# Optimization experiments

Hardware: AMD Instinct MI355X
Metric: run time of the kernel (lower is better)

Reference implementation:

```python
import jax, jax.numpy as jnp
import numpy as np

E = 8            # moe_num_experts
FFN = 8192       # ffn_hidden_size
D = 2048         # d_model
B, T = 1, 4096


def setup_inputs() -> dict:
    key = jax.random.key(0)
    k1, k2, k3, k4 = jax.random.split(key, 4)
    x = jax.random.normal(k1, (B, T, D), dtype=jnp.float32)
    # params stored flat as (E*FFN, D), as in the flax module
    w1 = jax.random.normal(k2, (E * FFN, D), dtype=jnp.float32) * 0.02
    v1 = jax.random.normal(k3, (E * FFN, D), dtype=jnp.float32) * 0.02
    w2 = jax.random.normal(k4, (E * FFN, D), dtype=jnp.float32) * 0.02
    return {"x": x, "w1": w1, "v1": v1, "w2": w2, "expert_idx": 3}


def reference(x, w1, v1, w2, expert_idx):
    # select this expert's weight slabs: (FFN, D) each
    expert_shape = (E, FFN, D)
    ew1 = w1.reshape(expert_shape)[expert_idx]
    ev1 = v1.reshape(expert_shape)[expert_idx]
    ew2 = w2.reshape(expert_shape)[expert_idx]
    # gate and up projections: [B,T,D] x [D,FFN] -> [B,T,FFN]
    x1 = jnp.einsum('btd,fd->btf', x, ew1)
    x2 = jnp.einsum('btd,fd->btf', x, ev1)
    h = jax.nn.silu(x1) * x2
    # down projection (note: matmul with ew2, i.e. contraction over FFN)
    out = jnp.einsum('btf,fd->btd', h, ew2)
    return out
```

## Files before the change

kernel.cpp:

```cpp
#include <hip/hip_runtime.h>

#define E_NUM 8
#define FFN_DIM 8192
#define D_DIM 2048
#define T_DIM 4096

using bf16x8 = __attribute__((ext_vector_type(8))) short;
using f32x4  = __attribute__((ext_vector_type(4))) float;
using u16x8  = __attribute__((ext_vector_type(8))) unsigned short;

__device__ __forceinline__ unsigned short f2bf(float f) {
  union { float f; unsigned int u; } v; v.f = f;
  unsigned int u = v.u;
  unsigned int r = (u + 0x7FFFu + ((u >> 16) & 1u)) >> 16;
  return (unsigned short)r;
}

__device__ __forceinline__ void gload16(const unsigned short* g, const unsigned short* l) {
  __builtin_amdgcn_global_load_lds(
      (const __attribute__((address_space(1))) void*)g,
      (__attribute__((address_space(3))) void*)l, 16, 0, 0);
}

__global__ void convert3_kernel(const float* __restrict__ x,
                                const float* __restrict__ w1,
                                const float* __restrict__ v1,
                                const int* __restrict__ eidx,
                                unsigned short* __restrict__ Xb,
                                unsigned short* __restrict__ W1b,
                                unsigned short* __restrict__ V1b) {
  const long slab = (long)FFN_DIM * D_DIM;
  const float* src;
  unsigned short* dst;
  long n;
  if (blockIdx.y == 0)      { src = w1 + (long)(*eidx) * slab; dst = W1b; n = slab; }
  else if (blockIdx.y == 1) { src = v1 + (long)(*eidx) * slab; dst = V1b; n = slab; }
  else                      { src = x;                          dst = Xb;  n = (long)T_DIM * D_DIM; }
  long stride = (long)gridDim.x * blockDim.x;
  for (long i = (long)blockIdx.x * blockDim.x + threadIdx.x; i * 8 < n; i += stride) {
    long e = i * 8;
    const float4* p = (const float4*)(src + e);
    float4 f0 = p[0], f1 = p[1];
    u16x8 o;
    o[0] = f2bf(f0.x); o[1] = f2bf(f0.y); o[2] = f2bf(f0.z); o[3] = f2bf(f0.w);
    o[4] = f2bf(f1.x); o[5] = f2bf(f1.y); o[6] = f2bf(f1.z); o[7] = f2bf(f1.w);
    *(u16x8*)(dst + e) = o;
  }
}

__global__ __launch_bounds__(512) void transpose_kernel(
    const float* __restrict__ w2, const int* __restrict__ eidx,
    unsigned short* __restrict__ dst) {
  __shared__ unsigned short tile[64][72];
  const float* src = w2 + (long)(*eidx) * (long)FFN_DIM * D_DIM;
  const int tid = threadIdx.x;
  int d0 = blockIdx.x << 6;
  int f0 = blockIdx.y << 6;
#pragma unroll
  for (int p = 0; p < 2; ++p) {
    int f = p * 32 + (tid >> 4);
    int dc = (tid & 15) * 4;
    float4 v = *(const float4*)(src + (long)(f0 + f) * D_DIM + d0 + dc);
    tile[f][dc + 0] = f2bf(v.x); tile[f][dc + 1] = f2bf(v.y);
    tile[f][dc + 2] = f2bf(v.z); tile[f][dc + 3] = f2bf(v.w);
  }
  __syncthreads();
  int d = tid >> 3;
  int fc = (tid & 7) * 8;
  u16x8 o;
#pragma unroll
  for (int j = 0; j < 8; ++j) o[j] = tile[fc + j][d];
  *(u16x8*)(dst + (long)(d0 + d) * FFN_DIM + f0 + fc) = o;
}

#define VMCNT6 asm volatile("s_waitcnt vmcnt(6)" ::: "memory")
#define VMCNT5 asm volatile("s_waitcnt vmcnt(5)" ::: "memory")
#define VMCNT3 asm volatile("s_waitcnt vmcnt(3)" ::: "memory")
#define VMCNT0 asm volatile("s_waitcnt vmcnt(0)" ::: "memory")
#define BAR asm volatile("s_waitcnt lgkmcnt(0)\n\ts_barrier" ::: "memory")
#define PRIO1 __builtin_amdgcn_s_setprio(1)
#define PRIO0 __builtin_amdgcn_s_setprio(0)

__global__ __launch_bounds__(512, 1) void gemm1_silu(
    const unsigned short* __restrict__ Xb,
    const unsigned short* __restrict__ W1b,
    const unsigned short* __restrict__ V1b,
    unsigned short* __restrict__ Hb) {
  __shared__ __align__(16) unsigned short sA[2 * 16384];
  __shared__ __align__(16) unsigned short sB1[2 * 8192];
  __shared__ __align__(16) unsigned short sB2[2 * 8192];

  const int tid = threadIdx.x;
  const int wv = tid >> 6, l = tid & 63;
  const int wm = wv >> 2, wn = wv & 3;
  const int kq = l >> 4, lr = l & 15;
  const int bsw = (blockIdx.x & 7) * 128 + (blockIdx.x >> 3);
  const int m0 = (bsw >> 6) << 8;
  const int n0 = (bsw & 63) << 7;

  const int rsub = tid >> 3;
  const int sslot8 = ((tid & 7) ^ ((tid >> 3) & 7)) << 3;
  const unsigned short* gA  = Xb  + (long)(m0 + rsub) * D_DIM + sslot8;
  const unsigned short* gB1 = W1b + (long)(n0 + rsub) * D_DIM + sslot8;
  const unsigned short* gB2 = V1b + (long)(n0 + rsub) * D_DIM + sslot8;

#define STG1(gbase, r_, tc_, lbase) \
  gload16((gbase) + (long)((r_) * 64) * D_DIM + (tc_), (lbase) + (r_) * 4096 + wv * 512)

  int aoffA[4], aoffB[4], boff[2];
#pragma unroll
  for (int j = 0; j < 4; ++j) {
    int rowA = wm * 64 + j * 16 + lr;
    aoffA[j] = rowA * 64 + ((kq ^ (rowA & 7)) << 3);
    int rowB = 128 + wm * 64 + j * 16 + lr;
    aoffB[j] = rowB * 64 + ((kq ^ (rowB & 7)) << 3);
  }
#pragma unroll
  for (int g = 0; g < 2; ++g) {
    int row = wn * 32 + g * 16 + lr;
    boff[g] = row * 64 + ((kq ^ (row & 7)) << 3);
  }

  f32x4 acc1[8][2], acc2[8][2];
  f32x4 z = {0.f, 0.f, 0.f, 0.f};
#pragma unroll
  for (int f = 0; f < 8; ++f)
#pragma unroll
    for (int g = 0; g < 2; ++g) { acc1[f][g] = z; acc2[f][g] = z; }

  bf16x8 aA[4][2], aB[4][2], b1[2][2], b2[2][2];

  STG1(gB1, 0, 0, sB1); STG1(gB1, 1, 0, sB1);
  STG1(gA, 0, 0, sA); STG1(gA, 1, 0, sA); STG1(gA, 2, 0, sA); STG1(gA, 3, 0, sA);
  STG1(gB2, 0, 0, sB2); STG1(gB2, 1, 0, sB2);
  STG1(gB1, 0, 64, sB1 + 8192); STG1(gB1, 1, 64, sB1 + 8192);
  STG1(gA, 0, 64, sA + 16384); STG1(gA, 1, 64, sA + 16384);
  STG1(gA, 2, 64, sA + 16384); STG1(gA, 3, 64, sA + 16384);
  STG1(gB2, 0, 64, sB2 + 8192); STG1(gB2, 1, 64, sB2 + 8192);
  asm volatile("s_waitcnt vmcnt(8)" ::: "memory");
  BAR;
#pragma unroll
  for (int j = 0; j < 4; ++j) {
    aA[j][0] = *(const bf16x8*)(sA + aoffA[j]);
    aA[j][1] = *(const bf16x8*)(sA + (aoffA[j] ^ 32));
  }
#pragma unroll
  for (int g = 0; g < 2; ++g) {
    b1[g][0] = *(const bf16x8*)(sB1 + boff[g]);
    b1[g][1] = *(const bf16x8*)(sB1 + (boff[g] ^ 32));
  }
  BAR;

  const int NT = D_DIM / 64;
  for (int t = 0; t < NT; ++t) {
    const int db = t & 1, nx = db ^ 1;
    const unsigned short* Acur  = sA  + db * 16384;
    const unsigned short* Anxt  = sA  + nx * 16384;
    const unsigned short* B1nxt = sB1 + nx * 8192;
    const unsigned short* B2cur = sB2 + db * 8192;
    unsigned short* AcurW  = (unsigned short*)sA  + db * 16384;
    unsigned short* B1curW = (unsigned short*)sB1 + db * 8192;
    unsigned short* B2curW = (unsigned short*)sB2 + db * 8192;
    const int p1ok = (t + 1 < NT), p2ok = (t + 2 < NT);
    const int tc2 = (t + 2) << 6;

#pragma unroll
    for (int j = 0; j < 4; ++j) {
      aB[j][0] = *(const bf16x8*)(Acur + aoffB[j]);
      aB[j][1] = *(const bf16x8*)(Acur + (aoffB[j] ^ 32));
    }
    if (p2ok) { STG1(gB1, 0, tc2, B1curW); STG1(gB1, 1, tc2, B1curW); }
    PRIO1;
#pragma unroll
    for (int j = 0; j < 4; ++j)
#pragma unroll
      for (int g = 0; g < 2; ++g) {
        acc1[j][g] = __builtin_amdgcn_mfma_f32_16x16x32_bf16(aA[j][0], b1[g][0], acc1[j][g], 0, 0, 0);
        acc1[j][g] = __builtin_amdgcn_mfma_f32_16x16x32_bf16(aA[j][1], b1[g][1], acc1[j][g], 0, 0, 0);
      }
    PRIO0;
    BAR;

#pragma unroll
    for (int g = 0; g < 2; ++g) {
      b2[g][0] = *(const bf16x8*)(B2cur + boff[g]);
      b2[g][1] = *(const bf16x8*)(B2cur + (boff[g] ^ 32));
    }
    if (p2ok) { STG1(gA, 0, tc2, AcurW); STG1(gA, 1, tc2, AcurW); STG1(gA, 2, tc2, AcurW); }
    PRIO1;
#pragma unroll
    for (int j = 0; j < 4; ++j)
#pragma unroll
      for (int g = 0; g < 2; ++g) {
        acc1[4 + j][g] = __builtin_amdgcn_mfma_f32_16x16x32_bf16(aB[j][0], b1[g][0], acc1[4 + j][g], 0, 0, 0);
        acc1[4 + j][g] = __builtin_amdgcn_mfma_f32_16x16x32_bf16(aB[j][1], b1[g][1], acc1[4 + j][g], 0, 0, 0);
      }
    PRIO0;
    if (p2ok) { VMCNT5; } else if (p1ok) { VMCNT0; }
    BAR;

    if (p2ok) { STG1(gA, 3, tc2, AcurW); STG1(gB2, 0, tc2, B2curW); STG1(gB2, 1, tc2, B2curW); }
    PRIO1;
#pragma unroll
    for (int j = 0; j < 4; ++j)
#pragma unroll
      for (int g = 0; g < 2; ++g) {
        acc2[j][g] = __builtin_amdgcn_mfma_f32_16x16x32_bf16(aA[j][0], b2[g][0], acc2[j][g], 0, 0, 0);
        acc2[j][g] = __builtin_amdgcn_mfma_f32_16x16x32_bf16(aA[j][1], b2[g][1], acc2[j][g], 0, 0, 0);
      }
    PRIO0;
    if (p1ok) {
#pragma unroll
      for (int j = 0; j < 4; ++j) {
        aA[j][0] = *(const bf16x8*)(Anxt + aoffA[j]);
        aA[j][1] = *(const bf16x8*)(Anxt + (aoffA[j] ^ 32));
      }
    }
    BAR;

    PRIO1;
#pragma unroll
    for (int j = 0; j < 4; ++j)
#pragma unroll
      for (int g = 0; g < 2; ++g) {
        acc2[4 + j][g] = __builtin_amdgcn_mfma_f32_16x16x32_bf16(aB[j][0], b2[g][0], acc2[4 + j][g], 0, 0, 0);
        acc2[4 + j][g] = __builtin_amdgcn_mfma_f32_16x16x32_bf16(aB[j][1], b2[g][1], acc2[4 + j][g], 0, 0, 0);
      }
    PRIO0;
    if (p1ok) {
#pragma unroll
      for (int g = 0; g < 2; ++g) {
        b1[g][0] = *(const bf16x8*)(B1nxt + boff[g]);
        b1[g][1] = *(const bf16x8*)(B1nxt + (boff[g] ^ 32));
      }
    }
    BAR;
  }

#pragma unroll
  for (int f = 0; f < 8; ++f)
#pragma unroll
    for (int g = 0; g < 2; ++g)
#pragma unroll
      for (int r = 0; r < 4; ++r) {
        int row = m0 + (f >> 2) * 128 + wm * 64 + (f & 3) * 16 + kq * 4 + r;
        int col = n0 + wn * 32 + g * 16 + lr;
        float x1 = acc1[f][g][r], x2 = acc2[f][g][r];
        float hv = x1 / (1.f + __expf(-x1)) * x2;
        Hb[(long)row * FFN_DIM + col] = f2bf(hv);
      }
#undef STG1
}

__global__ __launch_bounds__(512, 1) void gemm2(
    const unsigned short* __restrict__ Hb,
    const unsigned short* __restrict__ W2T,
    float* __restrict__ out) {
  __shared__ __align__(16) unsigned short sA[2 * 16384];
  __shared__ __align__(16) unsigned short sB[2 * 8192];

  const int tid = threadIdx.x;
  const int wv = tid >> 6, l = tid & 63;
  const int wm = wv >> 1, wn = wv & 1;
  const int kq = l >> 4, lr = l & 15;
  const int bsw = (blockIdx.x & 7) * 32 + (blockIdx.x >> 3);
  const int m0 = (bsw >> 4) << 8;
  const int n0 = (bsw & 15) << 7;

  const int rsub = tid >> 3;
  const int sslot8 = ((tid & 7) ^ ((tid >> 3) & 7)) << 3;
  const unsigned short* gA = Hb  + (long)(m0 + rsub) * FFN_DIM + sslot8;
  const unsigned short* gB = W2T + (long)(n0 + rsub) * FFN_DIM + sslot8;

#define STG1(gbase, r_, tc_, lbase) \
  gload16((gbase) + (long)((r_) * 64) * FFN_DIM + (tc_), (lbase) + (r_) * 4096 + wv * 512)

  int aoff[4], boff[4];
#pragma unroll
  for (int f = 0; f < 4; ++f) {
    int row = wm * 64 + f * 16 + lr;
    aoff[f] = row * 64 + ((kq ^ (row & 7)) << 3);
  }
#pragma unroll
  for (int g = 0; g < 4; ++g) {
    int row = wn * 64 + g * 16 + lr;
    boff[g] = row * 64 + ((kq ^ (row & 7)) << 3);
  }

  f32x4 acc[4][4];
  f32x4 z = {0.f, 0.f, 0.f, 0.f};
#pragma unroll
  for (int f = 0; f < 4; ++f)
#pragma unroll
    for (int g = 0; g < 4; ++g) acc[f][g] = z;

  bf16x8 aA[2][2], aB[2][2], bA[2][2], bB[2][2];

  STG1(gB, 0, 0, sB); STG1(gB, 1, 0, sB);
  STG1(gA, 0, 0, sA); STG1(gA, 1, 0, sA); STG1(gA, 2, 0, sA); STG1(gA, 3, 0, sA);
  STG1(gB, 0, 64, sB + 8192); STG1(gB, 1, 64, sB + 8192);
  STG1(gA, 0, 64, sA + 16384); STG1(gA, 1, 64, sA + 16384);
  STG1(gA, 2, 64, sA + 16384); STG1(gA, 3, 64, sA + 16384);
  VMCNT6;
  BAR;
#pragma unroll
  for (int f = 0; f < 2; ++f) {
    aA[f][0] = *(const bf16x8*)(sA + aoff[f]);
    aA[f][1] = *(const bf16x8*)(sA + (aoff[f] ^ 32));
  }
#pragma unroll
  for (int g = 0; g < 2; ++g) {
    bA[g][0] = *(const bf16x8*)(sB + boff[g]);
    bA[g][1] = *(const bf16x8*)(sB + (boff[g] ^ 32));
  }
  BAR;

  const int NT = FFN_DIM / 64;
  for (int t = 0; t < NT; ++t) {
    const int db = t & 1, nx = db ^ 1;
    const unsigned short* Acur = sA + db * 16384;
    const unsigned short* Anxt = sA + nx * 16384;
    const unsigned short* Bcur = sB + db * 8192;
    const unsigned short* Bnxt = sB + nx * 8192;
    unsigned short* AcurW = (unsigned short*)sA + db * 16384;
    unsigned short* BcurW = (unsigned short*)sB + db * 8192;
    const int p1ok = (t + 1 < NT), p2ok = (t + 2 < NT);
    const int tc2 = (t + 2) << 6;

#pragma unroll
    for (int f = 0; f < 2; ++f) {
      aB[f][0] = *(const bf16x8*)(Acur + aoff[2 + f]);
      aB[f][1] = *(const bf16x8*)(Acur + (aoff[2 + f] ^ 32));
    }
#pragma unroll
    for (int g = 0; g < 2; ++g) {
      bB[g][0] = *(const bf16x8*)(Bcur + boff[2 + g]);
      bB[g][1] = *(const bf16x8*)(Bcur + (boff[2 + g] ^ 32));
    }
    PRIO1;
#pragma unroll
    for (int f = 0; f < 2; ++f)
#pragma unroll
      for (int g = 0; g < 2; ++g) {
        acc[f][g] = __builtin_amdgcn_mfma_f32_16x16x32_bf16(aA[f][0], bA[g][0], acc[f][g], 0, 0, 0);
        acc[f][g] = __builtin_amdgcn_mfma_f32_16x16x32_bf16(aA[f][1], bA[g][1], acc[f][g], 0, 0, 0);
      }
    PRIO0;
    BAR;

    if (p2ok) { STG1(gB, 0, tc2, BcurW); STG1(gB, 1, tc2, BcurW); STG1(gA, 0, tc2, AcurW); }
    PRIO1;
#pragma unroll
    for (int f = 0; f < 2; ++f)
#pragma unroll
      for (int g = 0; g < 2; ++g) {
        acc[2 + f][g] = __builtin_amdgcn_mfma_f32_16x16x32_bf16(aB[f][0], bA[g][0], acc[2 + f][g], 0, 0, 0);
        acc[2 + f][g] = __builtin_amdgcn_mfma_f32_16x16x32_bf16(aB[f][1], bA[g][1], acc[2 + f][g], 0, 0, 0);
      }
    PRIO0;
    if (p2ok) { VMCNT3; } else if (p1ok) { VMCNT0; }
    BAR;

    if (p2ok) { STG1(gA, 1, tc2, AcurW); STG1(gA, 2, tc2, AcurW); STG1(gA, 3, tc2, AcurW); }
    PRIO1;
#pragma unroll
    for (int f = 0; f < 2; ++f)
#pragma unroll
      for (int g = 0; g < 2; ++g) {
        acc[f][2 + g] = __builtin_amdgcn_mfma_f32_16x16x32_bf16(aA[f][0], bB[g][0], acc[f][2 + g], 0, 0, 0);
        acc[f][2 + g] = __builtin_amdgcn_mfma_f32_16x16x32_bf16(aA[f][1], bB[g][1], acc[f][2 + g], 0, 0, 0);
      }
    PRIO0;
    if (p1ok) {
#pragma unroll
      for (int f = 0; f < 2; ++f) {
        aA[f][0] = *(const bf16x8*)(Anxt + aoff[f]);
        aA[f][1] = *(const bf16x8*)(Anxt + (aoff[f] ^ 32));
      }
    }
    BAR;

    PRIO1;
#pragma unroll
    for (int f = 0; f < 2; ++f)
#pragma unroll
      for (int g = 0; g < 2; ++g) {
        acc[2 + f][2 + g] = __builtin_amdgcn_mfma_f32_16x16x32_bf16(aB[f][0], bB[g][0], acc[2 + f][2 + g], 0, 0, 0);
        acc[2 + f][2 + g] = __builtin_amdgcn_mfma_f32_16x16x32_bf16(aB[f][1], bB[g][1], acc[2 + f][2 + g], 0, 0, 0);
      }
    PRIO0;
    if (p1ok) {
#pragma unroll
      for (int g = 0; g < 2; ++g) {
        bA[g][0] = *(const bf16x8*)(Bnxt + boff[g]);
        bA[g][1] = *(const bf16x8*)(Bnxt + (boff[g] ^ 32));
      }
    }
    BAR;
  }

#pragma unroll
  for (int f = 0; f < 4; ++f)
#pragma unroll
    for (int g = 0; g < 4; ++g)
#pragma unroll
      for (int r = 0; r < 4; ++r) {
        int row = m0 + wm * 64 + f * 16 + kq * 4 + r;
        int col = n0 + wn * 64 + g * 16 + lr;
        out[(long)row * D_DIM + col] = acc[f][g][r];
      }
#undef STG1
}

extern "C" void kernel_launch(void* const* d_in, const int* in_sizes, int n_in,
                              void* d_out, int out_size, void* d_ws, size_t ws_size,
                              hipStream_t stream) {
  const float* x  = (const float*)d_in[0];
  const float* w1 = (const float*)d_in[1];
  const float* v1 = (const float*)d_in[2];
  const float* w2 = (const float*)d_in[3];
  const int* eidx = (const int*)d_in[4];

  char* ws = (char*)d_ws;
  unsigned short* Xb  = (unsigned short*)(ws);
  unsigned short* W1b = (unsigned short*)(ws + (16l << 20));
  unsigned short* V1b = (unsigned short*)(ws + (48l << 20));
  unsigned short* W2T = (unsigned short*)(ws + (80l << 20));
  unsigned short* Hb  = (unsigned short*)(ws + (112l << 20));
  float* out = (float*)d_out;

  transpose_kernel<<<dim3(D_DIM / 64, FFN_DIM / 64), 512, 0, stream>>>(w2, eidx, W2T);
  convert3_kernel<<<dim3(2048, 3), 256, 0, stream>>>(x, w1, v1, eidx, Xb, W1b, V1b);
  gemm1_silu<<<1024, 512, 0, stream>>>(Xb, W1b, V1b, Hb);
  gemm2<<<256, 512, 0, stream>>>(Hb, W2T, out);
}
```

Measured before the change: 483.1 us.

## Reschedule gemm1 prefetch stages and relax LDS waits at barriers

```diff
diff --git a/kernel.cpp b/kernel.cpp
--- a/kernel.cpp
+++ b/kernel.cpp
@@ -73,10 +73,14 @@
   *(u16x8*)(dst + (long)(d0 + d) * FFN_DIM + f0 + fc) = o;
 }
 
+#define VMCNT8 asm volatile("s_waitcnt vmcnt(8)" ::: "memory")
 #define VMCNT6 asm volatile("s_waitcnt vmcnt(6)" ::: "memory")
-#define VMCNT5 asm volatile("s_waitcnt vmcnt(5)" ::: "memory")
+#define VMCNT4 asm volatile("s_waitcnt vmcnt(4)" ::: "memory")
 #define VMCNT3 asm volatile("s_waitcnt vmcnt(3)" ::: "memory")
 #define VMCNT0 asm volatile("s_waitcnt vmcnt(0)" ::: "memory")
+#define LGKM8 asm volatile("s_waitcnt lgkmcnt(8)" ::: "memory")
+#define LGKM4 asm volatile("s_waitcnt lgkmcnt(4)" ::: "memory")
+#define BARP  asm volatile("s_barrier" ::: "memory")
 #define BAR asm volatile("s_waitcnt lgkmcnt(0)\n\ts_barrier" ::: "memory")
 #define PRIO1 __builtin_amdgcn_s_setprio(1)
 #define PRIO0 __builtin_amdgcn_s_setprio(0)
@@ -137,8 +141,8 @@
   STG1(gA, 0, 64, sA + 16384); STG1(gA, 1, 64, sA + 16384);
   STG1(gA, 2, 64, sA + 16384); STG1(gA, 3, 64, sA + 16384);
   STG1(gB2, 0, 64, sB2 + 8192); STG1(gB2, 1, 64, sB2 + 8192);
-  asm volatile("s_waitcnt vmcnt(8)" ::: "memory");
-  BAR;
+  VMCNT8;
+  BARP;
 #pragma unroll
   for (int j = 0; j < 4; ++j) {
     aA[j][0] = *(const bf16x8*)(sA + aoffA[j]);
@@ -158,9 +162,9 @@
     const unsigned short* Anxt  = sA  + nx * 16384;
     const unsigned short* B1nxt = sB1 + nx * 8192;
     const unsigned short* B2cur = sB2 + db * 8192;
-    unsigned short* AcurW  = (unsigned short*)sA  + db * 16384;
-    unsigned short* B1curW = (unsigned short*)sB1 + db * 8192;
-    unsigned short* B2curW = (unsigned short*)sB2 + db * 8192;
+    unsigned short* AdbW  = (unsigned short*)sA  + db * 16384;
+    unsigned short* B1dbW = (unsigned short*)sB1 + db * 8192;
+    unsigned short* B2dbW = (unsigned short*)sB2 + db * 8192;
     const int p1ok = (t + 1 < NT), p2ok = (t + 2 < NT);
     const int tc2 = (t + 2) << 6;
 
@@ -169,7 +173,6 @@
       aB[j][0] = *(const bf16x8*)(Acur + aoffB[j]);
       aB[j][1] = *(const bf16x8*)(Acur + (aoffB[j] ^ 32));
     }
-    if (p2ok) { STG1(gB1, 0, tc2, B1curW); STG1(gB1, 1, tc2, B1curW); }
     PRIO1;
 #pragma unroll
     for (int j = 0; j < 4; ++j)
@@ -179,14 +182,15 @@
         acc1[j][g] = __builtin_amdgcn_mfma_f32_16x16x32_bf16(aA[j][1], b1[g][1], acc1[j][g], 0, 0, 0);
       }
     PRIO0;
-    BAR;
+    LGKM8;
+    BARP;
 
 #pragma unroll
     for (int g = 0; g < 2; ++g) {
       b2[g][0] = *(const bf16x8*)(B2cur + boff[g]);
       b2[g][1] = *(const bf16x8*)(B2cur + (boff[g] ^ 32));
     }
-    if (p2ok) { STG1(gA, 0, tc2, AcurW); STG1(gA, 1, tc2, AcurW); STG1(gA, 2, tc2, AcurW); }
+    if (p2ok) { STG1(gB1, 0, tc2, B1dbW); STG1(gB1, 1, tc2, B1dbW); }
     PRIO1;
 #pragma unroll
     for (int j = 0; j < 4; ++j)
@@ -196,10 +200,12 @@
         acc1[4 + j][g] = __builtin_amdgcn_mfma_f32_16x16x32_bf16(aB[j][1], b1[g][1], acc1[4 + j][g], 0, 0, 0);
       }
     PRIO0;
-    if (p2ok) { VMCNT5; } else if (p1ok) { VMCNT0; }
-    BAR;
-
-    if (p2ok) { STG1(gA, 3, tc2, AcurW); STG1(gB2, 0, tc2, B2curW); STG1(gB2, 1, tc2, B2curW); }
+    if (p2ok) { VMCNT4; } else { VMCNT0; }
+    LGKM4;
+    BARP;
+
+    if (p2ok) { STG1(gA, 0, tc2, AdbW); STG1(gA, 1, tc2, AdbW);
+                STG1(gA, 2, tc2, AdbW); STG1(gA, 3, tc2, AdbW); }
     PRIO1;
 #pragma unroll
     for (int j = 0; j < 4; ++j)
@@ -216,8 +222,10 @@
         aA[j][1] = *(const bf16x8*)(Anxt + (aoffA[j] ^ 32));
       }
     }
-    BAR;
-
+    LGKM8;
+    BARP;
+
+    if (p2ok) { STG1(gB2, 0, tc2, B2dbW); STG1(gB2, 1, tc2, B2dbW); }
     PRIO1;
 #pragma unroll
     for (int j = 0; j < 4; ++j)
@@ -234,7 +242,9 @@
         b1[g][1] = *(const bf16x8*)(B1nxt + (boff[g] ^ 32));
       }
     }
-    BAR;
+    if (p2ok) { VMCNT8; } else { VMCNT0; }
+    LGKM4;
+    BARP;
   }
 
 #pragma unroll
```

Result: slower. 530.3 us (+9.8%).

## Merge prep kernels into one launch and retile gemm2 to 128x128 with 2 blocks/CU

Applied to the files above, without the earlier changes.

```diff
diff --git a/kernel.cpp b/kernel.cpp
--- a/kernel.cpp
+++ b/kernel.cpp
@@ -22,14 +22,38 @@
       (__attribute__((address_space(3))) void*)l, 16, 0, 0);
 }
 
-__global__ void convert3_kernel(const float* __restrict__ x,
-                                const float* __restrict__ w1,
-                                const float* __restrict__ v1,
-                                const int* __restrict__ eidx,
-                                unsigned short* __restrict__ Xb,
-                                unsigned short* __restrict__ W1b,
-                                unsigned short* __restrict__ V1b) {
+__global__ __launch_bounds__(512) void prep4_kernel(
+    const float* __restrict__ x,  const float* __restrict__ w1,
+    const float* __restrict__ v1, const float* __restrict__ w2,
+    const int* __restrict__ eidx,
+    unsigned short* __restrict__ Xb,  unsigned short* __restrict__ W1b,
+    unsigned short* __restrict__ V1b, unsigned short* __restrict__ W2T) {
+  __shared__ unsigned short tile[64][72];
   const long slab = (long)FFN_DIM * D_DIM;
+  const int tid = threadIdx.x;
+
+  if (blockIdx.y == 3) {
+    const float* src = w2 + (long)(*eidx) * slab;
+    int d0 = (blockIdx.x & 31) << 6;
+    int f0 = (blockIdx.x >> 5) << 6;
+#pragma unroll
+    for (int p = 0; p < 2; ++p) {
+      int f = p * 32 + (tid >> 4);
+      int dc = (tid & 15) * 4;
+      float4 v = *(const float4*)(src + (long)(f0 + f) * D_DIM + d0 + dc);
+      tile[f][dc + 0] = f2bf(v.x); tile[f][dc + 1] = f2bf(v.y);
+      tile[f][dc + 2] = f2bf(v.z); tile[f][dc + 3] = f2bf(v.w);
+    }
+    __syncthreads();
+    int d = tid >> 3;
+    int fc = (tid & 7) * 8;
+    u16x8 o;
+#pragma unroll
+    for (int j = 0; j < 8; ++j) o[j] = tile[fc + j][d];
+    *(u16x8*)(W2T + (long)(d0 + d) * FFN_DIM + f0 + fc) = o;
+    return;
+  }
+
   const float* src;
   unsigned short* dst;
   long n;
@@ -37,7 +61,7 @@
   else if (blockIdx.y == 1) { src = v1 + (long)(*eidx) * slab; dst = V1b; n = slab; }
   else                      { src = x;                          dst = Xb;  n = (long)T_DIM * D_DIM; }
   long stride = (long)gridDim.x * blockDim.x;
-  for (long i = (long)blockIdx.x * blockDim.x + threadIdx.x; i * 8 < n; i += stride) {
+  for (long i = (long)blockIdx.x * blockDim.x + tid; i * 8 < n; i += stride) {
     long e = i * 8;
     const float4* p = (const float4*)(src + e);
     float4 f0 = p[0], f1 = p[1];
@@ -48,34 +72,8 @@
   }
 }
 
-__global__ __launch_bounds__(512) void transpose_kernel(
-    const float* __restrict__ w2, const int* __restrict__ eidx,
-    unsigned short* __restrict__ dst) {
-  __shared__ unsigned short tile[64][72];
-  const float* src = w2 + (long)(*eidx) * (long)FFN_DIM * D_DIM;
-  const int tid = threadIdx.x;
-  int d0 = blockIdx.x << 6;
-  int f0 = blockIdx.y << 6;
-#pragma unroll
-  for (int p = 0; p < 2; ++p) {
-    int f = p * 32 + (tid >> 4);
-    int dc = (tid & 15) * 4;
-    float4 v = *(const float4*)(src + (long)(f0 + f) * D_DIM + d0 + dc);
-    tile[f][dc + 0] = f2bf(v.x); tile[f][dc + 1] = f2bf(v.y);
-    tile[f][dc + 2] = f2bf(v.z); tile[f][dc + 3] = f2bf(v.w);
-  }
-  __syncthreads();
-  int d = tid >> 3;
-  int fc = (tid & 7) * 8;
-  u16x8 o;
-#pragma unroll
-  for (int j = 0; j < 8; ++j) o[j] = tile[fc + j][d];
-  *(u16x8*)(dst + (long)(d0 + d) * FFN_DIM + f0 + fc) = o;
-}
-
-#define VMCNT6 asm volatile("s_waitcnt vmcnt(6)" ::: "memory")
+#define VMCNT8 asm volatile("s_waitcnt vmcnt(8)" ::: "memory")
 #define VMCNT5 asm volatile("s_waitcnt vmcnt(5)" ::: "memory")
-#define VMCNT3 asm volatile("s_waitcnt vmcnt(3)" ::: "memory")
 #define VMCNT0 asm volatile("s_waitcnt vmcnt(0)" ::: "memory")
 #define BAR asm volatile("s_waitcnt lgkmcnt(0)\n\ts_barrier" ::: "memory")
 #define PRIO1 __builtin_amdgcn_s_setprio(1)
@@ -137,7 +135,7 @@
   STG1(gA, 0, 64, sA + 16384); STG1(gA, 1, 64, sA + 16384);
   STG1(gA, 2, 64, sA + 16384); STG1(gA, 3, 64, sA + 16384);
   STG1(gB2, 0, 64, sB2 + 8192); STG1(gB2, 1, 64, sB2 + 8192);
-  asm volatile("s_waitcnt vmcnt(8)" ::: "memory");
+  VMCNT8;
   BAR;
 #pragma unroll
   for (int j = 0; j < 4; ++j) {
@@ -252,28 +250,28 @@
 #undef STG1
 }
 
-__global__ __launch_bounds__(512, 1) void gemm2(
+__global__ __launch_bounds__(256, 2) void gemm2(
     const unsigned short* __restrict__ Hb,
     const unsigned short* __restrict__ W2T,
     float* __restrict__ out) {
-  __shared__ __align__(16) unsigned short sA[2 * 16384];
+  __shared__ __align__(16) unsigned short sA[2 * 8192];
   __shared__ __align__(16) unsigned short sB[2 * 8192];
 
   const int tid = threadIdx.x;
   const int wv = tid >> 6, l = tid & 63;
   const int wm = wv >> 1, wn = wv & 1;
   const int kq = l >> 4, lr = l & 15;
-  const int bsw = (blockIdx.x & 7) * 32 + (blockIdx.x >> 3);
-  const int m0 = (bsw >> 4) << 8;
+  const int bsw = (blockIdx.x & 7) * 64 + (blockIdx.x >> 3);
+  const int m0 = (bsw >> 4) << 7;
   const int n0 = (bsw & 15) << 7;
 
   const int rsub = tid >> 3;
-  const int sslot8 = ((tid & 7) ^ ((tid >> 3) & 7)) << 3;
+  const int sslot8 = ((tid & 7) ^ (rsub & 7)) << 3;
   const unsigned short* gA = Hb  + (long)(m0 + rsub) * FFN_DIM + sslot8;
   const unsigned short* gB = W2T + (long)(n0 + rsub) * FFN_DIM + sslot8;
 
-#define STG1(gbase, r_, tc_, lbase) \
-  gload16((gbase) + (long)((r_) * 64) * FFN_DIM + (tc_), (lbase) + (r_) * 4096 + wv * 512)
+#define STG2(gbase, r_, tc_, lbase) \
+  gload16((gbase) + (long)((r_) * 32) * FFN_DIM + (tc_), (lbase) + (r_) * 2048 + wv * 512)
 
   int aoff[4], boff[4];
 #pragma unroll
@@ -294,107 +292,54 @@
 #pragma unroll
     for (int g = 0; g < 4; ++g) acc[f][g] = z;
 
-  bf16x8 aA[2][2], aB[2][2], bA[2][2], bB[2][2];
-
-  STG1(gB, 0, 0, sB); STG1(gB, 1, 0, sB);
-  STG1(gA, 0, 0, sA); STG1(gA, 1, 0, sA); STG1(gA, 2, 0, sA); STG1(gA, 3, 0, sA);
-  STG1(gB, 0, 64, sB + 8192); STG1(gB, 1, 64, sB + 8192);
-  STG1(gA, 0, 64, sA + 16384); STG1(gA, 1, 64, sA + 16384);
-  STG1(gA, 2, 64, sA + 16384); STG1(gA, 3, 64, sA + 16384);
-  VMCNT6;
-  BAR;
-#pragma unroll
-  for (int f = 0; f < 2; ++f) {
-    aA[f][0] = *(const bf16x8*)(sA + aoff[f]);
-    aA[f][1] = *(const bf16x8*)(sA + (aoff[f] ^ 32));
-  }
-#pragma unroll
-  for (int g = 0; g < 2; ++g) {
-    bA[g][0] = *(const bf16x8*)(sB + boff[g]);
-    bA[g][1] = *(const bf16x8*)(sB + (boff[g] ^ 32));
-  }
+  STG2(gA, 0, 0, sA); STG2(gA, 1, 0, sA); STG2(gA, 2, 0, sA); STG2(gA, 3, 0, sA);
+  STG2(gB, 0, 0, sB); STG2(gB, 1, 0, sB); STG2(gB, 2, 0, sB); STG2(gB, 3, 0, sB);
+  STG2(gA, 0, 64, sA + 8192); STG2(gA, 1, 64, sA + 8192);
+  STG2(gA, 2, 64, sA + 8192); STG2(gA, 3, 64, sA + 8192);
+  STG2(gB, 0, 64, sB + 8192); STG2(gB, 1, 64, sB + 8192);
+  STG2(gB, 2, 64, sB + 8192); STG2(gB, 3, 64, sB + 8192);
+  VMCNT8;
   BAR;
 
   const int NT = FFN_DIM / 64;
   for (int t = 0; t < NT; ++t) {
-    const int db = t & 1, nx = db ^ 1;
-    const unsigned short* Acur = sA + db * 16384;
-    const unsigned short* Anxt = sA + nx * 16384;
-    const unsigned short* Bcur = sB + db * 8192;
-    const unsigned short* Bnxt = sB + nx * 8192;
-    unsigned short* AcurW = (unsigned short*)sA + db * 16384;
-    unsigned short* BcurW = (unsigned short*)sB + db * 8192;
-    const int p1ok = (t + 1 < NT), p2ok = (t + 2 < NT);
-    const int tc2 = (t + 2) << 6;
-
-#pragma unroll
-    for (int f = 0; f < 2; ++f) {
-      aB[f][0] = *(const bf16x8*)(Acur + aoff[2 + f]);
-      aB[f][1] = *(const bf16x8*)(Acur + (aoff[2 + f] ^ 32));
-    }
-#pragma unroll
-    for (int g = 0; g < 2; ++g) {
-      bB[g][0] = *(const bf16x8*)(Bcur + boff[2 + g]);
-      bB[g][1] = *(const bf16x8*)(Bcur + (boff[2 + g] ^ 32));
-    }
-    PRIO1;
-#pragma unroll
-    for (int f = 0; f < 2; ++f)
-#pragma unroll
-      for (int g = 0; g < 2; ++g) {
-        acc[f][g] = __builtin_amdgcn_mfma_f32_16x16x32_bf16(aA[f][0], bA[g][0], acc[f][g], 0, 0, 0);
-        acc[f][g] = __builtin_amdgcn_mfma_f32_16x16x32_bf16(aA[f][1], bA[g][1], acc[f][g], 0, 0, 0);
-      }
-    PRIO0;
-    BAR;
-
-    if (p2ok) { STG1(gB, 0, tc2, BcurW); STG1(gB, 1, tc2, BcurW); STG1(gA, 0, tc2, AcurW); }
-    PRIO1;
-#pragma unroll
-    for (int f = 0; f < 2; ++f)
-#pragma unroll
-      for (int g = 0; g < 2; ++g) {
-        acc[2 + f][g] = __builtin_amdgcn_mfma_f32_16x16x32_bf16(aB[f][0], bA[g][0], acc[2 + f][g], 0, 0, 0);
-        acc[2 + f][g] = __builtin_amdgcn_mfma_f32_16x16x32_bf16(aB[f][1], bA[g][1], acc[2 + f][g], 0, 0, 0);
-      }
-    PRIO0;
-    if (p2ok) { VMCNT3; } else if (p1ok) { VMCNT0; }
-    BAR;
-
-    if (p2ok) { STG1(gA, 1, tc2, AcurW); STG1(gA, 2, tc2, AcurW); STG1(gA, 3, tc2, AcurW); }
-    PRIO1;
-#pragma unroll
-    for (int f = 0; f < 2; ++f)
-#pragma unroll
-      for (int g = 0; g < 2; ++g) {
-        acc[f][2 + g] = __builtin_amdgcn_mfma_f32_16x16x32_bf16(aA[f][0], bB[g][0], acc[f][2 + g], 0, 0, 0);
-        acc[f][2 + g] = __builtin_amdgcn_mfma_f32_16x16x32_bf16(aA[f][1], bB[g][1], acc[f][2 + g], 0, 0, 0);
-      }
-    PRIO0;
-    if (p1ok) {
-#pragma unroll
-      for (int f = 0; f < 2; ++f) {
-        aA[f][0] = *(const bf16x8*)(Anxt + aoff[f]);
-        aA[f][1] = *(const bf16x8*)(Anxt + (aoff[f] ^ 32));
-      }
-    }
-    BAR;
-
-    PRIO1;
-#pragma unroll
-    for (int f = 0; f < 2; ++f)
-#pragma unroll
-      for (int g = 0; g < 2; ++g) {
-        acc[2 + f][2 + g] = __builtin_amdgcn_mfma_f32_16x16x32_bf16(aB[f][0], bB[g][0], acc[2 + f][2 + g], 0, 0, 0);
-        acc[2 + f][2 + g] = __builtin_amdgcn_mfma_f32_16x16x32_bf16(aB[f][1], bB[g][1], acc[2 + f][2 + g], 0, 0, 0);
-      }
-    PRIO0;
-    if (p1ok) {
-#pragma unroll
-      for (int g = 0; g < 2; ++g) {
-        bA[g][0] = *(const bf16x8*)(Bnxt + boff[g]);
-        bA[g][1] = *(const bf16x8*)(Bnxt + (boff[g] ^ 32));
-      }
+    const int cur = t & 1;
+    const unsigned short* Ac = sA + cur * 8192;
+    const unsigned short* Bc = sB + cur * 8192;
+    unsigned short* AcW = (unsigned short*)sA + cur * 8192;
+    unsigned short* BcW = (unsigned short*)sB + cur * 8192;
+    bf16x8 af[4][2], bf_[4][2];
+
+#pragma unroll
+    for (int f = 0; f < 4; ++f) {
+      af[f][0] = *(const bf16x8*)(Ac + aoff[f]);
+      af[f][1] = *(const bf16x8*)(Ac + (aoff[f] ^ 32));
+    }
+#pragma unroll
+    for (int g = 0; g < 4; ++g) {
+      bf_[g][0] = *(const bf16x8*)(Bc + boff[g]);
+      bf_[g][1] = *(const bf16x8*)(Bc + (boff[g] ^ 32));
+    }
+    PRIO1;
+#pragma unroll
+    for (int f = 0; f < 4; ++f)
+#pragma unroll
+      for (int g = 0; g < 4; ++g) {
+        acc[f][g] = __builtin_amdgcn_mfma_f32_16x16x32_bf16(af[f][0], bf_[g][0], acc[f][g], 0, 0, 0);
+        acc[f][g] = __builtin_amdgcn_mfma_f32_16x16x32_bf16(af[f][1], bf_[g][1], acc[f][g], 0, 0, 0);
+      }
+    PRIO0;
+    BAR;
+
+    if (t + 2 < NT) {
+      const int tc2 = (t + 2) << 6;
+      STG2(gA, 0, tc2, AcW); STG2(gA, 1, tc2, AcW);
+      STG2(gA, 2, tc2, AcW); STG2(gA, 3, tc2, AcW);
+      STG2(gB, 0, tc2, BcW); STG2(gB, 1, tc2, BcW);
+      STG2(gB, 2, tc2, BcW); STG2(gB, 3, tc2, BcW);
+      VMCNT8;
+    } else if (t + 1 < NT) {
+      VMCNT0;
     }
     BAR;
   }
@@ -409,7 +354,7 @@
         int col = n0 + wn * 64 + g * 16 + lr;
         out[(long)row * D_DIM + col] = acc[f][g][r];
       }
-#undef STG1
+#undef STG2
 }
 
 extern "C" void kernel_launch(void* const* d_in, const int* in_sizes, int n_in,
@@ -429,8 +374,7 @@
   unsigned short* Hb  = (unsigned short*)(ws + (112l << 20));
   float* out = (float*)d_out;
 
-  transpose_kernel<<<dim3(D_DIM / 64, FFN_DIM / 64), 512, 0, stream>>>(w2, eidx, W2T);
-  convert3_kernel<<<dim3(2048, 3), 256, 0, stream>>>(x, w1, v1, eidx, Xb, W1b, V1b);
+  prep4_kernel<<<dim3(4096, 4), 512, 0, stream>>>(x, w1, v1, w2, eidx, Xb, W1b, V1b, W2T);
   gemm1_silu<<<1024, 512, 0, stream>>>(Xb, W1b, V1b, Hb);
-  gemm2<<<256, 512, 0, stream>>>(Hb, W2T, out);
-}
+  gemm2<<<512, 256, 0, stream>>>(Hb, W2T, out);
+}
```

Result: faster. 440.1 us, median of 2 (-8.9%).
